# Performance work log

Hardware: AMD Instinct MI355X
Metric: run time of the kernel (lower is better)

The kernel has to match this reference:

```python
import jax, jax.numpy as jnp
import numpy as np

B, T, D = 4, 2048, 1024
H, KD, VD = 16, 64, 64  # num_heads, key_dim, value_dim; H*KD == D


def setup_inputs() -> dict:
    key = jax.random.key(0)
    ks = jax.random.split(key, 10)
    s = 0.02
    return {
        "q_in": jax.random.normal(ks[0], (B, T, D), jnp.float32),
        "v_in": jax.random.normal(ks[1], (B, T, D), jnp.float32),
        "Wq": jax.random.normal(ks[2], (D, H * KD), jnp.float32) * s,
        "bq": jnp.zeros((H * KD,), jnp.float32),
        "Wk": jax.random.normal(ks[3], (D, H * KD), jnp.float32) * s,
        "bk": jnp.zeros((H * KD,), jnp.float32),
        "Wv": jax.random.normal(ks[4], (D, H * VD), jnp.float32) * s,
        "bv": jnp.zeros((H * VD,), jnp.float32),
        "Wo": jax.random.normal(ks[5], (H * VD, D), jnp.float32) * s,
        "bo": jnp.zeros((D,), jnp.float32),
    }


def reference(q_in, v_in, Wq, bq, Wk, bk, Wv, bv, Wo, bo):
    # QKV projections (key defaults to value input)
    q = q_in @ Wq + bq                      # [B,T,H*KD]
    k = v_in @ Wk + bk                      # [B,T,H*KD]
    v = v_in @ Wv + bv                      # [B,T,H*VD]
    q = q.reshape(B, T, H, KD)
    k = k.reshape(B, T, H, KD)
    v = v.reshape(B, T, H, VD)
    # scaled dot-product attention, scores materialized as [B,H,Tq,Tv]
    q = q / jnp.sqrt(jnp.asarray(KD, q.dtype))
    scores = jnp.einsum('bqnh,bvnh->bnqv', q, k)
    weights = jax.nn.softmax(scores, axis=-1)
    out = jnp.einsum('bnqv,bvnh->bqnh', weights, v)  # [B,Tq,H,VD]
    out = out.reshape(B, T, H * VD)
    return out @ Wo + bo                    # [B,T,D]
```

## Files before the change

kernel.cpp:

```cpp
#include <hip/hip_runtime.h>

#define BATCH  4
#define T_SEQ  2048
#define NH     16
#define DMODEL 1024
#define HD     64

typedef float    f32x4 __attribute__((ext_vector_type(4)));
typedef _Float16 f16x8 __attribute__((ext_vector_type(8)));
typedef _Float16 f16x4 __attribute__((ext_vector_type(4)));
typedef __fp16   h16x2 __attribute__((ext_vector_type(2)));

#define LOG2E 1.44269504088896f

__device__ __forceinline__ void lds_load16(const void* g, void* l) {
  __builtin_amdgcn_global_load_lds((const __attribute__((address_space(1))) void*)g,
                                   (__attribute__((address_space(3))) void*)l, 16, 0, 0);
}

__device__ __forceinline__ f16x4 pack4_f16(float a, float b, float c, float d) {
  union { h16x2 h[2]; f16x4 f; } u;
  u.h[0] = __builtin_amdgcn_cvt_pkrtz(a, b);
  u.h[1] = __builtin_amdgcn_cvt_pkrtz(c, d);
  return u.f;
}

__global__ __launch_bounds__(256) void cast2_f32_to_f16(
    const float* __restrict__ a, const float* __restrict__ bsrc,
    _Float16* __restrict__ oa, _Float16* __restrict__ ob, int n4) {
  const float* in = blockIdx.y ? bsrc : a;
  _Float16* out = blockIdx.y ? ob : oa;
  int i = blockIdx.x * 256 + threadIdx.x;
  if (i < n4) {
    float4 v = ((const float4*)in)[i];
    f16x4 o = { (_Float16)v.x, (_Float16)v.y, (_Float16)v.z, (_Float16)v.w };
    ((f16x4*)out)[i] = o;
  }
}

__global__ __launch_bounds__(256) void transcast_w4(
    const float* __restrict__ W0, const float* __restrict__ W1,
    const float* __restrict__ W2, const float* __restrict__ W3,
    _Float16* __restrict__ T0, _Float16* __restrict__ T1,
    _Float16* __restrict__ T2, _Float16* __restrict__ T3) {
  const float* W; _Float16* Wt;
  switch (blockIdx.z) {
    case 0: W = W0; Wt = T0; break;
    case 1: W = W1; Wt = T1; break;
    case 2: W = W2; Wt = T2; break;
    default: W = W3; Wt = T3; break;
  }
  __shared__ float L[64][65];
  const int n0 = blockIdx.x * 64, k0 = blockIdx.y * 64;
  const int tx = threadIdx.x & 15, ty = threadIdx.x >> 4;
#pragma unroll
  for (int i = 0; i < 4; ++i) {
    float4 v = *(const float4*)&W[(size_t)(k0 + ty + 16 * i) * DMODEL + n0 + tx * 4];
    L[ty + 16 * i][tx * 4 + 0] = v.x;
    L[ty + 16 * i][tx * 4 + 1] = v.y;
    L[ty + 16 * i][tx * 4 + 2] = v.z;
    L[ty + 16 * i][tx * 4 + 3] = v.w;
  }
  __syncthreads();
#pragma unroll
  for (int i = 0; i < 4; ++i) {
    int n = n0 + ty + 16 * i;
    f16x4 o;
#pragma unroll
    for (int j = 0; j < 4; ++j) o[j] = (_Float16)L[tx * 4 + j][ty + 16 * i];
    *(f16x4*)&Wt[(size_t)n * DMODEL + k0 + tx * 4] = o;
  }
}

__device__ __forceinline__ void gemm97_body(
    const _Float16* __restrict__ A, const _Float16* __restrict__ Wt,
    const float* __restrict__ bias, void* __restrict__ Cout, float scale,
    int mode, _Float16* As, _Float16* Bs) {
  const int K = DMODEL;
  const int lane = threadIdx.x & 63, wave = threadIdx.x >> 6;
  const int bid = blockIdx.x + blockIdx.y * gridDim.x;
  const int m0 = ((bid & 7) * 8 + ((bid >> 3) & 7)) * 128;
  const int n0 = (bid >> 6) * 128;
  const int wr = (wave & 1) * 4;
  const int wc = (wave >> 1) * 4;
  const int m16 = lane & 15, quad = lane >> 4;

  const _Float16* ap[4]; const _Float16* bp[4];
#pragma unroll
  for (int j = 0; j < 4; ++j) {
    int g = wave * 4 + j;
    ap[j] = A  + (size_t)(m0 + (g >> 1) * 16 + m16) * K + (g & 1) * 32 + quad * 8;
    bp[j] = Wt + (size_t)(n0 + (g >> 1) * 16 + m16) * K + (g & 1) * 32 + quad * 8;
  }

  f32x4 acc[4][4] = {};

  for (int k0 = 0; k0 < 1024; k0 += 64) {
    __syncthreads();
#pragma unroll
    for (int j = 0; j < 4; ++j) {
      lds_load16(ap[j] + k0, As + (wave * 4 + j) * 512);
      lds_load16(bp[j] + k0, Bs + (wave * 4 + j) * 512);
    }
    __syncthreads();
#pragma unroll
    for (int s = 0; s < 2; ++s) {
      f16x8 bf[4];
#pragma unroll
      for (int ni = 0; ni < 4; ++ni)
        bf[ni] = *(const f16x8*)(Bs + (((wc + ni) * 2 + s) * 64 + lane) * 8);
#pragma unroll
      for (int mi = 0; mi < 4; ++mi) {
        f16x8 af = *(const f16x8*)(As + (((wr + mi) * 2 + s) * 64 + lane) * 8);
#pragma unroll
        for (int ni = 0; ni < 4; ++ni)
          acc[mi][ni] = __builtin_amdgcn_mfma_f32_16x16x32_f16(af, bf[ni], acc[mi][ni], 0, 0, 0);
      }
    }
  }

  if (mode == 2) {
#pragma unroll
    for (int mi = 0; mi < 4; ++mi)
#pragma unroll
      for (int ni = 0; ni < 4; ++ni) {
        int row = m0 + (wr + mi) * 16 + quad * 4;
        int col = n0 + (wc + ni) * 16 + m16;
        int bb = row >> 11, tt = row & (T_SEQ - 1);
        int hh = col >> 6, dd = col & 63;
        float bv = bias[col];
        f16x4 pv = pack4_f16(acc[mi][ni][0] + bv, acc[mi][ni][1] + bv,
                             acc[mi][ni][2] + bv, acc[mi][ni][3] + bv);
        *(f16x4*)&((_Float16*)Cout)[(((size_t)bb * NH + hh) * HD + dd) * T_SEQ + tt] = pv;
      }
  } else if (mode == 0) {
#pragma unroll
    for (int mi = 0; mi < 4; ++mi)
#pragma unroll
      for (int r = 0; r < 4; ++r) {
        int row = m0 + (wr + mi) * 16 + quad * 4 + r;
#pragma unroll
        for (int ni = 0; ni < 4; ++ni) {
          int col = n0 + (wc + ni) * 16 + m16;
          float v = (acc[mi][ni][r] + bias[col]) * scale;
          ((_Float16*)Cout)[(size_t)row * DMODEL + col] = (_Float16)v;
        }
      }
  } else {
#pragma unroll
    for (int mi = 0; mi < 4; ++mi)
#pragma unroll
      for (int r = 0; r < 4; ++r) {
        int row = m0 + (wr + mi) * 16 + quad * 4 + r;
#pragma unroll
        for (int ni = 0; ni < 4; ++ni) {
          int col = n0 + (wc + ni) * 16 + m16;
          ((float*)Cout)[(size_t)row * DMODEL + col] = acc[mi][ni][r] + bias[col];
        }
      }
  }
}

__global__ __launch_bounds__(256, 3) void gemm_qkv(
    const _Float16* __restrict__ Aq, const _Float16* __restrict__ Av,
    const _Float16* __restrict__ Wq, const _Float16* __restrict__ Wk,
    const _Float16* __restrict__ Wv,
    const float* __restrict__ bq, const float* __restrict__ bk,
    const float* __restrict__ bv,
    _Float16* __restrict__ Cq, _Float16* __restrict__ Ck, _Float16* __restrict__ Cv) {
  __shared__ _Float16 As[128 * 64], Bs[128 * 64];
  const _Float16* A; const _Float16* Wt; const float* bias; _Float16* C;
  float scale; int mode;
  if (blockIdx.z == 0)      { A = Aq; Wt = Wq; bias = bq; C = Cq; scale = 0.125f * LOG2E; mode = 0; }
  else if (blockIdx.z == 1) { A = Av; Wt = Wk; bias = bk; C = Ck; scale = 1.f; mode = 0; }
  else                      { A = Av; Wt = Wv; bias = bv; C = Cv; scale = 1.f; mode = 2; }
  gemm97_body(A, Wt, bias, C, scale, mode, As, Bs);
}

__global__ __launch_bounds__(256, 3) void gemm_out(
    const _Float16* __restrict__ A, const _Float16* __restrict__ Wt,
    const float* __restrict__ bias, float* __restrict__ Cout) {
  __shared__ _Float16 As[128 * 64], Bs[128 * 64];
  gemm97_body(A, Wt, bias, Cout, 1.f, 3, As, Bs);
}

__global__ __launch_bounds__(256, 2) void attn_mfma(
    const _Float16* __restrict__ Q, const _Float16* __restrict__ Kb,
    const _Float16* __restrict__ Vt, _Float16* __restrict__ O) {
  __shared__ _Float16 Ks[64 * 64], Vs[64 * 64];
  __shared__ _Float16 Ps[4 * 4096];

  const int lane = threadIdx.x & 63, wave = threadIdx.x >> 6;
  const int m16 = lane & 15, quad = lane >> 4;
  const int h = blockIdx.x;
  const int q0 = blockIdx.y * 256;
  const int b = blockIdx.z;
  const int wq = wave * 64;
  const int wbase = wave * 4096;

  f16x8 qf[4][2];
#pragma unroll
  for (int mi = 0; mi < 4; ++mi)
#pragma unroll
    for (int ki = 0; ki < 2; ++ki) {
      int q = q0 + wq + mi * 16 + m16;
      qf[mi][ki] = *(const f16x8*)(Q + (((size_t)b * T_SEQ + q) * NH + h) * HD + ki * 32 + quad * 8);
    }

  const _Float16 *kp[2], *vp[2];
#pragma unroll
  for (int i = 0; i < 2; ++i) {
    int g = wave * 128 + i * 64 + lane;
    int tk = (g >> 7) * 16 + (g & 15);
    int dkof = ((g >> 6) & 1) * 32 + ((g >> 4) & 3) * 8;
    kp[i] = Kb + (((size_t)b * T_SEQ + tk) * NH + h) * HD + dkof;
    int dvof = (g >> 7) * 16 + (g & 15);
    int tv = ((g >> 6) & 1) * 32 + ((g >> 4) & 3) * 8;
    vp[i] = Vt + (((size_t)b * NH + h) * HD + dvof) * T_SEQ + tv;
  }

  int pw[4][4];
#pragma unroll
  for (int mi = 0; mi < 4; ++mi)
#pragma unroll
    for (int nt = 0; nt < 4; ++nt) {
      int kt = nt >> 1;
      int q8 = ((nt & 1) << 1) | (quad >> 1);
      pw[mi][nt] = wbase + ((mi * 2 + kt) * 64 + q8 * 16 + m16) * 8 + (quad & 1) * 4;
    }

  const f16x8 onef = {(_Float16)1, (_Float16)1, (_Float16)1, (_Float16)1,
                      (_Float16)1, (_Float16)1, (_Float16)1, (_Float16)1};

  f32x4 o_acc[4][4] = {};
  f32x4 l_acc[4] = {};

  for (int kv = 0; kv < T_SEQ; kv += 64) {
    __syncthreads();
#pragma unroll
    for (int i = 0; i < 2; ++i) {
      lds_load16(kp[i] + (size_t)kv * (NH * HD), Ks + (wave * 2 + i) * 512);
      lds_load16(vp[i] + kv, Vs + (wave * 2 + i) * 512);
    }
    __syncthreads();

    f32x4 st[4][4] = {};
#pragma unroll
    for (int nt = 0; nt < 4; ++nt)
#pragma unroll
      for (int ki = 0; ki < 2; ++ki) {
        f16x8 kf = *(const f16x8*)(Ks + ((nt * 2 + ki) * 64 + lane) * 8);
#pragma unroll
        for (int mi = 0; mi < 4; ++mi)
          st[mi][nt] = __builtin_amdgcn_mfma_f32_16x16x32_f16(kf, qf[mi][ki], st[mi][nt], 0, 0, 0);
      }

#pragma unroll
    for (int mi = 0; mi < 4; ++mi)
#pragma unroll
      for (int nt = 0; nt < 4; ++nt) {
        f16x4 p = pack4_f16(__builtin_amdgcn_exp2f(st[mi][nt][0]),
                            __builtin_amdgcn_exp2f(st[mi][nt][1]),
                            __builtin_amdgcn_exp2f(st[mi][nt][2]),
                            __builtin_amdgcn_exp2f(st[mi][nt][3]));
        *(f16x4*)(Ps + pw[mi][nt]) = p;
      }

#pragma unroll
    for (int kt = 0; kt < 2; ++kt) {
      f16x8 pf[4];
#pragma unroll
      for (int mi = 0; mi < 4; ++mi) {
        pf[mi] = *(const f16x8*)(Ps + wbase + ((mi * 2 + kt) * 64 + lane) * 8);
        l_acc[mi] = __builtin_amdgcn_mfma_f32_16x16x32_f16(pf[mi], onef, l_acc[mi], 0, 0, 0);
      }
#pragma unroll
      for (int nd = 0; nd < 4; ++nd) {
        f16x8 vf = *(const f16x8*)(Vs + ((nd * 2 + kt) * 64 + lane) * 8);
#pragma unroll
        for (int mi = 0; mi < 4; ++mi)
          o_acc[mi][nd] = __builtin_amdgcn_mfma_f32_16x16x32_f16(pf[mi], vf, o_acc[mi][nd], 0, 0, 0);
      }
    }
  }

#pragma unroll
  for (int mi = 0; mi < 4; ++mi)
#pragma unroll
    for (int r = 0; r < 4; ++r) {
      float inv = 1.f / l_acc[mi][r];
      int q = q0 + wq + mi * 16 + quad * 4 + r;
#pragma unroll
      for (int nd = 0; nd < 4; ++nd) {
        int d = nd * 16 + m16;
        O[(((size_t)b * T_SEQ + q) * NH + h) * HD + d] = (_Float16)(o_acc[mi][nd][r] * inv);
      }
    }
}

extern "C" void kernel_launch(void* const* d_in, const int* in_sizes, int n_in,
                              void* d_out, int out_size, void* d_ws, size_t ws_size,
                              hipStream_t stream) {
  const float* q_in = (const float*)d_in[0];
  const float* v_in = (const float*)d_in[1];
  const float* Wq   = (const float*)d_in[2];
  const float* bq   = (const float*)d_in[3];
  const float* Wk   = (const float*)d_in[4];
  const float* bk   = (const float*)d_in[5];
  const float* Wv   = (const float*)d_in[6];
  const float* bv   = (const float*)d_in[7];
  const float* Wo   = (const float*)d_in[8];
  const float* bo   = (const float*)d_in[9];
  float* out = (float*)d_out;

  const size_t MB = 1u << 20;
  char* ws = (char*)d_ws;
  _Float16* q16  = (_Float16*)(ws);
  _Float16* v16  = (_Float16*)(ws + 16 * MB);
  _Float16* qbuf = (_Float16*)(ws + 32 * MB);
  _Float16* kbuf = (_Float16*)(ws + 48 * MB);
  _Float16* vtb  = (_Float16*)(ws + 64 * MB);
  _Float16* Wqt  = (_Float16*)(ws + 80 * MB);
  _Float16* Wkt  = (_Float16*)(ws + 82 * MB);
  _Float16* Wvt  = (_Float16*)(ws + 84 * MB);
  _Float16* Wot  = (_Float16*)(ws + 86 * MB);

  const int n4 = BATCH * T_SEQ * DMODEL / 4;
  cast2_f32_to_f16<<<dim3(n4 / 256, 2), 256, 0, stream>>>(q_in, v_in, q16, v16, n4);

  transcast_w4<<<dim3(16, 16, 4), 256, 0, stream>>>(Wq, Wk, Wv, Wo, Wqt, Wkt, Wvt, Wot);

  gemm_qkv<<<dim3(8, 64, 3), 256, 0, stream>>>(q16, v16, Wqt, Wkt, Wvt, bq, bk, bv,
                                               qbuf, kbuf, vtb);

  attn_mfma<<<dim3(16, 8, 4), 256, 0, stream>>>(qbuf, kbuf, vtb, qbuf);

  gemm_out<<<dim3(8, 64), 256, 0, stream>>>(qbuf, Wot, bo, out);
}
```

Before: 343.0 us.

## Rewrite projection GEMMs as 256x256 tiles with double-buffered LDS pipeline

```diff
diff --git a/kernel.cpp b/kernel.cpp
--- a/kernel.cpp
+++ b/kernel.cpp
@@ -24,6 +24,13 @@
   u.h[1] = __builtin_amdgcn_cvt_pkrtz(c, d);
   return u.f;
 }
+
+#define MEMFENCE asm volatile("" ::: "memory")
+#define WAITVM4  asm volatile("s_waitcnt vmcnt(4)" ::: "memory")
+#define WAITVM0  asm volatile("s_waitcnt vmcnt(0)" ::: "memory")
+#define PH_ENTER do { MEMFENCE; __builtin_amdgcn_s_barrier(); \
+                      asm volatile("s_waitcnt lgkmcnt(0)" ::: "memory"); } while (0)
+#define PH_EXIT  do { MEMFENCE; __builtin_amdgcn_s_barrier(); MEMFENCE; } while (0)
 
 __global__ __launch_bounds__(256) void cast2_f32_to_f16(
     const float* __restrict__ a, const float* __restrict__ bsrc,
@@ -72,116 +79,189 @@
   }
 }
 
-__device__ __forceinline__ void gemm97_body(
+__device__ __forceinline__ void gemm256_body(
     const _Float16* __restrict__ A, const _Float16* __restrict__ Wt,
     const float* __restrict__ bias, void* __restrict__ Cout, float scale,
-    int mode, _Float16* As, _Float16* Bs) {
+    int mode, _Float16* As0, _Float16* Bs0, _Float16* As1, _Float16* Bs1) {
   const int K = DMODEL;
   const int lane = threadIdx.x & 63, wave = threadIdx.x >> 6;
-  const int bid = blockIdx.x + blockIdx.y * gridDim.x;
-  const int m0 = ((bid & 7) * 8 + ((bid >> 3) & 7)) * 128;
-  const int n0 = (bid >> 6) * 128;
-  const int wr = (wave & 1) * 4;
-  const int wc = (wave >> 1) * 4;
   const int m16 = lane & 15, quad = lane >> 4;
-
-  const _Float16* ap[4]; const _Float16* bp[4];
-#pragma unroll
-  for (int j = 0; j < 4; ++j) {
-    int g = wave * 4 + j;
-    ap[j] = A  + (size_t)(m0 + (g >> 1) * 16 + m16) * K + (g & 1) * 32 + quad * 8;
-    bp[j] = Wt + (size_t)(n0 + (g >> 1) * 16 + m16) * K + (g & 1) * 32 + quad * 8;
-  }
-
-  f32x4 acc[4][4] = {};
-
-  for (int k0 = 0; k0 < 1024; k0 += 64) {
-    __syncthreads();
-#pragma unroll
-    for (int j = 0; j < 4; ++j) {
-      lds_load16(ap[j] + k0, As + (wave * 4 + j) * 512);
-      lds_load16(bp[j] + k0, Bs + (wave * 4 + j) * 512);
-    }
-    __syncthreads();
-#pragma unroll
-    for (int s = 0; s < 2; ++s) {
-      f16x8 bf[4];
-#pragma unroll
-      for (int ni = 0; ni < 4; ++ni)
-        bf[ni] = *(const f16x8*)(Bs + (((wc + ni) * 2 + s) * 64 + lane) * 8);
-#pragma unroll
-      for (int mi = 0; mi < 4; ++mi) {
-        f16x8 af = *(const f16x8*)(As + (((wr + mi) * 2 + s) * 64 + lane) * 8);
-#pragma unroll
-        for (int ni = 0; ni < 4; ++ni)
-          acc[mi][ni] = __builtin_amdgcn_mfma_f32_16x16x32_f16(af, bf[ni], acc[mi][ni], 0, 0, 0);
-      }
-    }
-  }
+  const int wm = wave & 1;
+  const int wn = wave >> 1;
+
+  const int lin = blockIdx.x + blockIdx.y * gridDim.x;
+  const int wg = (lin & 7) * 16 + (lin >> 3);
+  const int m0 = (wg >> 2) * 256;
+  const int n0 = (wg & 3) * 256;
+
+  const int kof = (wave & 1) * 32 + quad * 8;
+  const _Float16* aB[2][2]; const _Float16* bB[2][2];
+#pragma unroll
+  for (int h = 0; h < 2; ++h)
+#pragma unroll
+    for (int j = 0; j < 2; ++j) {
+      int r = h * 128 + (wave >> 1) * 16 + 64 * j + m16;
+      aB[h][j] = A  + (size_t)(m0 + r) * K + kof;
+      bB[h][j] = Wt + (size_t)(n0 + r) * K + kof;
+    }
+
+  auto stageA = [&](_Float16* Ab, int h, int t) {
+#pragma unroll
+    for (int j = 0; j < 2; ++j)
+      lds_load16(aB[h][j] + t * 64, Ab + (h * 16 + wave + 8 * j) * 512 + lane * 8);
+  };
+  auto stageB = [&](_Float16* Bb, int h, int t) {
+#pragma unroll
+    for (int j = 0; j < 2; ++j)
+      lds_load16(bB[h][j] + t * 64, Bb + (h * 16 + wave + 8 * j) * 512 + lane * 8);
+  };
+  auto rdA = [&](const _Float16* Ab, int mi, int kh) {
+    return *(const f16x8*)(Ab + (((wm * 8 + mi) * 2 + kh) * 64 + lane) * 8);
+  };
+  auto rdB = [&](const _Float16* Bb, int ni, int kh) {
+    return *(const f16x8*)(Bb + (((wn * 4 + ni) * 2 + kh) * 64 + lane) * 8);
+  };
+
+  f32x4 acc[8][4] = {};
+
+  auto tile_step = [&](int t, _Float16* Ac, const _Float16* Bc, _Float16* Bn) {
+    f16x8 a03[4][2], a47[4][2], b01[2][2], b23[2][2];
+#pragma unroll
+    for (int mi = 0; mi < 4; ++mi) { a03[mi][0] = rdA(Ac, mi, 0); a03[mi][1] = rdA(Ac, mi, 1); }
+#pragma unroll
+    for (int ni = 0; ni < 2; ++ni) { b01[ni][0] = rdB(Bc, ni, 0); b01[ni][1] = rdB(Bc, ni, 1); }
+    if (t < 15) stageB(Bn, 0, t + 1);
+    PH_ENTER;
+    __builtin_amdgcn_s_setprio(1);
+#pragma unroll
+    for (int mi = 0; mi < 4; ++mi)
+#pragma unroll
+      for (int ni = 0; ni < 2; ++ni)
+#pragma unroll
+        for (int kh = 0; kh < 2; ++kh)
+          acc[mi][ni] = __builtin_amdgcn_mfma_f32_16x16x32_f16(a03[mi][kh], b01[ni][kh], acc[mi][ni], 0, 0, 0);
+    __builtin_amdgcn_s_setprio(0);
+    PH_EXIT;
+#pragma unroll
+    for (int ni = 0; ni < 2; ++ni) { b23[ni][0] = rdB(Bc, 2 + ni, 0); b23[ni][1] = rdB(Bc, 2 + ni, 1); }
+    if (t < 15) stageB(Bn, 1, t + 1);
+    PH_ENTER;
+    __builtin_amdgcn_s_setprio(1);
+#pragma unroll
+    for (int mi = 0; mi < 4; ++mi)
+#pragma unroll
+      for (int ni = 0; ni < 2; ++ni)
+#pragma unroll
+        for (int kh = 0; kh < 2; ++kh)
+          acc[mi][2 + ni] = __builtin_amdgcn_mfma_f32_16x16x32_f16(a03[mi][kh], b23[ni][kh], acc[mi][2 + ni], 0, 0, 0);
+    __builtin_amdgcn_s_setprio(0);
+    PH_EXIT;
+#pragma unroll
+    for (int mi = 0; mi < 4; ++mi) { a47[mi][0] = rdA(Ac, 4 + mi, 0); a47[mi][1] = rdA(Ac, 4 + mi, 1); }
+    PH_ENTER;
+    __builtin_amdgcn_s_setprio(1);
+#pragma unroll
+    for (int mi = 0; mi < 4; ++mi)
+#pragma unroll
+      for (int ni = 0; ni < 2; ++ni)
+#pragma unroll
+        for (int kh = 0; kh < 2; ++kh)
+          acc[4 + mi][ni] = __builtin_amdgcn_mfma_f32_16x16x32_f16(a47[mi][kh], b01[ni][kh], acc[4 + mi][ni], 0, 0, 0);
+    __builtin_amdgcn_s_setprio(0);
+    PH_EXIT;
+    if (t < 14) { stageA(Ac, 0, t + 2); stageA(Ac, 1, t + 2); }
+    PH_ENTER;
+    __builtin_amdgcn_s_setprio(1);
+#pragma unroll
+    for (int mi = 0; mi < 4; ++mi)
+#pragma unroll
+      for (int ni = 0; ni < 2; ++ni)
+#pragma unroll
+        for (int kh = 0; kh < 2; ++kh)
+          acc[4 + mi][2 + ni] = __builtin_amdgcn_mfma_f32_16x16x32_f16(a47[mi][kh], b23[ni][kh], acc[4 + mi][2 + ni], 0, 0, 0);
+    __builtin_amdgcn_s_setprio(0);
+    if (t < 14)       WAITVM4;
+    else if (t == 14) WAITVM0;
+    MEMFENCE; __builtin_amdgcn_s_barrier(); MEMFENCE;
+  };
+
+  stageA(As0, 0, 0); stageA(As0, 1, 0);
+  stageB(Bs0, 0, 0); stageB(Bs0, 1, 0);
+  stageA(As1, 0, 1); stageA(As1, 1, 1);
+  WAITVM4;
+  MEMFENCE; __builtin_amdgcn_s_barrier(); MEMFENCE;
+
+  for (int tp = 0; tp < 8; ++tp) {
+    tile_step(2 * tp,     As0, Bs0, Bs1);
+    tile_step(2 * tp + 1, As1, Bs1, Bs0);
+  }
+
+  float bv[4];
+#pragma unroll
+  for (int ni = 0; ni < 4; ++ni) bv[ni] = bias[n0 + wn * 64 + ni * 16 + m16];
 
   if (mode == 2) {
 #pragma unroll
-    for (int mi = 0; mi < 4; ++mi)
+    for (int mi = 0; mi < 8; ++mi)
 #pragma unroll
       for (int ni = 0; ni < 4; ++ni) {
-        int row = m0 + (wr + mi) * 16 + quad * 4;
-        int col = n0 + (wc + ni) * 16 + m16;
+        int row = m0 + wm * 128 + mi * 16 + quad * 4;
+        int col = n0 + wn * 64 + ni * 16 + m16;
         int bb = row >> 11, tt = row & (T_SEQ - 1);
         int hh = col >> 6, dd = col & 63;
-        float bv = bias[col];
-        f16x4 pv = pack4_f16(acc[mi][ni][0] + bv, acc[mi][ni][1] + bv,
-                             acc[mi][ni][2] + bv, acc[mi][ni][3] + bv);
+        f16x4 pv = pack4_f16(acc[mi][ni][0] + bv[ni], acc[mi][ni][1] + bv[ni],
+                             acc[mi][ni][2] + bv[ni], acc[mi][ni][3] + bv[ni]);
         *(f16x4*)&((_Float16*)Cout)[(((size_t)bb * NH + hh) * HD + dd) * T_SEQ + tt] = pv;
       }
   } else if (mode == 0) {
 #pragma unroll
-    for (int mi = 0; mi < 4; ++mi)
+    for (int mi = 0; mi < 8; ++mi)
 #pragma unroll
       for (int r = 0; r < 4; ++r) {
-        int row = m0 + (wr + mi) * 16 + quad * 4 + r;
+        int row = m0 + wm * 128 + mi * 16 + quad * 4 + r;
 #pragma unroll
         for (int ni = 0; ni < 4; ++ni) {
-          int col = n0 + (wc + ni) * 16 + m16;
-          float v = (acc[mi][ni][r] + bias[col]) * scale;
+          int col = n0 + wn * 64 + ni * 16 + m16;
+          float v = (acc[mi][ni][r] + bv[ni]) * scale;
           ((_Float16*)Cout)[(size_t)row * DMODEL + col] = (_Float16)v;
         }
       }
   } else {
 #pragma unroll
-    for (int mi = 0; mi < 4; ++mi)
+    for (int mi = 0; mi < 8; ++mi)
 #pragma unroll
       for (int r = 0; r < 4; ++r) {
-        int row = m0 + (wr + mi) * 16 + quad * 4 + r;
+        int row = m0 + wm * 128 + mi * 16 + quad * 4 + r;
 #pragma unroll
         for (int ni = 0; ni < 4; ++ni) {
-          int col = n0 + (wc + ni) * 16 + m16;
-          ((float*)Cout)[(size_t)row * DMODEL + col] = acc[mi][ni][r] + bias[col];
+          int col = n0 + wn * 64 + ni * 16 + m16;
+          ((float*)Cout)[(size_t)row * DMODEL + col] = acc[mi][ni][r] + bv[ni];
         }
       }
   }
 }
 
-__global__ __launch_bounds__(256, 3) void gemm_qkv(
+__global__ __launch_bounds__(512, 2) void gemm_qkv(
     const _Float16* __restrict__ Aq, const _Float16* __restrict__ Av,
     const _Float16* __restrict__ Wq, const _Float16* __restrict__ Wk,
     const _Float16* __restrict__ Wv,
     const float* __restrict__ bq, const float* __restrict__ bk,
     const float* __restrict__ bv,
     _Float16* __restrict__ Cq, _Float16* __restrict__ Ck, _Float16* __restrict__ Cv) {
-  __shared__ _Float16 As[128 * 64], Bs[128 * 64];
+  __shared__ _Float16 As[2][16384], Bs[2][16384];
   const _Float16* A; const _Float16* Wt; const float* bias; _Float16* C;
   float scale; int mode;
   if (blockIdx.z == 0)      { A = Aq; Wt = Wq; bias = bq; C = Cq; scale = 0.125f * LOG2E; mode = 0; }
   else if (blockIdx.z == 1) { A = Av; Wt = Wk; bias = bk; C = Ck; scale = 1.f; mode = 0; }
   else                      { A = Av; Wt = Wv; bias = bv; C = Cv; scale = 1.f; mode = 2; }
-  gemm97_body(A, Wt, bias, C, scale, mode, As, Bs);
-}
-
-__global__ __launch_bounds__(256, 3) void gemm_out(
+  gemm256_body(A, Wt, bias, C, scale, mode, As[0], Bs[0], As[1], Bs[1]);
+}
+
+__global__ __launch_bounds__(512, 2) void gemm_out(
     const _Float16* __restrict__ A, const _Float16* __restrict__ Wt,
     const float* __restrict__ bias, float* __restrict__ Cout) {
-  __shared__ _Float16 As[128 * 64], Bs[128 * 64];
-  gemm97_body(A, Wt, bias, Cout, 1.f, 3, As, Bs);
+  __shared__ _Float16 As[2][16384], Bs[2][16384];
+  gemm256_body(A, Wt, bias, Cout, 1.f, 3, As[0], Bs[0], As[1], Bs[1]);
 }
 
 __global__ __launch_bounds__(256, 2) void attn_mfma(
@@ -330,10 +410,10 @@
 
   transcast_w4<<<dim3(16, 16, 4), 256, 0, stream>>>(Wq, Wk, Wv, Wo, Wqt, Wkt, Wvt, Wot);
 
-  gemm_qkv<<<dim3(8, 64, 3), 256, 0, stream>>>(q16, v16, Wqt, Wkt, Wvt, bq, bk, bv,
+  gemm_qkv<<<dim3(4, 32, 3), 512, 0, stream>>>(q16, v16, Wqt, Wkt, Wvt, bq, bk, bv,
                                                qbuf, kbuf, vtb);
 
   attn_mfma<<<dim3(16, 8, 4), 256, 0, stream>>>(qbuf, kbuf, vtb, qbuf);
 
-  gemm_out<<<dim3(8, 64), 256, 0, stream>>>(qbuf, Wot, bo, out);
-}
+  gemm_out<<<dim3(4, 32), 512, 0, stream>>>(qbuf, Wot, bo, out);
+}
```

Measured after the change: 337.8 us. About the same (-1.5%).
